# Kernel optimization log

Measured on AMD Instinct MI355X. Metric: run time of the kernel, lower is better.

## Reference

```python
import jax, jax.numpy as jnp
import numpy as np

N_NODES = 50000
N_EDGES = 150000
N_TRIS = 100000
F = 256
L = 4


def setup_inputs() -> dict:
    key = jax.random.key(0)
    ks = jax.random.split(key, 8)
    x = jax.random.normal(ks[0], (N_EDGES, F), dtype=jnp.float32)
    edge_nodes = jax.random.randint(ks[1], (N_EDGES, 2), 0, N_NODES)
    tri_edges = jax.random.randint(ks[2], (N_TRIS, 3), 0, N_EDGES)
    tri_signs = (jax.random.randint(ks[3], (N_TRIS, 3), 0, 2) * 2 - 1).astype(jnp.int32)
    std = float(np.sqrt(2.0 / (F + F)))  # xavier_uniform-equivalent std
    W0_stack = jax.random.normal(ks[4], (L, F, F), dtype=jnp.float32) * std
    W1_stack = jax.random.normal(ks[5], (L, F, F), dtype=jnp.float32) * std
    W2_stack = jax.random.normal(ks[6], (L, F, F), dtype=jnp.float32) * std
    W0_L = jax.random.normal(ks[7], (F, 1), dtype=jnp.float32) * float(np.sqrt(2.0 / (F + 1)))
    return {"x": x, "W0_stack": W0_stack, "W1_stack": W1_stack, "W2_stack": W2_stack,
            "W0_L": W0_L, "edge_nodes": edge_nodes, "tri_edges": tri_edges, "tri_signs": tri_signs}


def _b1_mm(edge_nodes, y):
    # B1 @ y : [E,F] -> [N,F];  B1[u,e] = -1, B1[v,e] = +1
    u, v = edge_nodes[:, 0], edge_nodes[:, 1]
    out = jnp.zeros((N_NODES, y.shape[1]), y.dtype)
    return out.at[u].add(-y).at[v].add(y)


def _b1t_mm(edge_nodes, z):
    # B1.T @ z : [N,F] -> [E,F]
    return z[edge_nodes[:, 1]] - z[edge_nodes[:, 0]]


def _b2t_mm(tri_edges, signs, y):
    # B2.T @ y : [E,F] -> [T,F]
    return jnp.einsum('tkf,tk->tf', y[tri_edges], signs)


def _b2_mm(tri_edges, signs, w):
    # B2 @ w : [T,F] -> [E,F]
    contrib = w[:, None, :] * signs[:, :, None]  # [T,3,F]
    out = jnp.zeros((N_EDGES, w.shape[1]), w.dtype)
    return out.at[tri_edges.reshape(-1)].add(contrib.reshape(-1, w.shape[1]))


def reference(x, W0_stack, W1_stack, W2_stack, W0_L, edge_nodes, tri_edges, tri_signs):
    signs = tri_signs.astype(x.dtype)
    for i in range(L):
        d2 = _b2_mm(tri_edges, signs, _b2t_mm(tri_edges, signs, x @ W2_stack[i]))
        d1 = x @ W1_stack[i]
        d0 = _b1t_mm(edge_nodes, _b1_mm(edge_nodes, x @ W0_stack[i]))
        x = jax.nn.relu(d2 + d1 + d0)
    return _b1_mm(edge_nodes, x @ W0_L)  # [N_NODES, 1]
```

## Files before the change

### kernel.cpp

```cpp
#include <hip/hip_runtime.h>

#define M_EDGES 150000
#define NN_NODES 50000
#define N_TRIS  100000
#define F 256
#define NLAYERS 4

#define T0 1172
#define T1 391
#define T2 782
#define NTILES (T0 + T1 + T2)
#define NT_PAD 2352
#define TPX 294

typedef __attribute__((ext_vector_type(8))) __bf16 bf16x8;
typedef __attribute__((ext_vector_type(4))) float f32x4;

__device__ inline unsigned short f2bf(float f) {
    unsigned int u = __float_as_uint(f);
    u += 0x7fff + ((u >> 16) & 1);
    return (unsigned short)(u >> 16);
}
__device__ inline float bf2f(unsigned short h) {
    return __uint_as_float(((unsigned int)h) << 16);
}

__device__ inline void async16(const void* g, void* l) {
    __builtin_amdgcn_global_load_lds(
        (const __attribute__((address_space(1))) void*)g,
        (__attribute__((address_space(3))) void*)l, 16, 0, 0);
}

__global__ __launch_bounds__(512) void gemm_mfma(
    const unsigned short* __restrict__ xb,
    const unsigned short* __restrict__ sb,
    const unsigned short* __restrict__ qb,
    const unsigned short* __restrict__ wt,
    unsigned short* __restrict__ y1,
    unsigned short* __restrict__ zb,
    unsigned short* __restrict__ wb)
{
    __shared__ unsigned short As[128 * 32];
    __shared__ unsigned short Bs[256 * 32];

    const int b    = blockIdx.x;
    const int xcd  = b & 7;
    const int idx  = b >> 3;
    const int tile = xcd * TPX + idx;
    if (tile >= NTILES) return;

    int seg, tloc;
    if (tile < T0)            { seg = 0; tloc = tile; }
    else if (tile < T0 + T1)  { seg = 1; tloc = tile - T0; }
    else                      { seg = 2; tloc = tile - T0 - T1; }
    const unsigned short* Asrc = (seg == 0) ? xb : (seg == 1) ? sb : qb;
    const int nrows = (seg == 0) ? M_EDGES : (seg == 1) ? NN_NODES : N_TRIS;
    const unsigned short* wsel = wt + seg * 65536;
    unsigned short* dst = (seg == 0) ? y1 : (seg == 1) ? zb : wb;

    const int tid  = threadIdx.x;
    const int bm0  = tloc * 128;
    const int wid  = tid >> 6;
    const int lane = tid & 63;
    const int lm   = lane & 15;
    const int lh   = lane >> 4;
    const int wm   = wid >> 2;
    const int wn   = wid & 3;
    const int wbase = tid & ~63;

    f32x4 cacc[4][4];
#pragma unroll
    for (int i = 0; i < 4; i++)
#pragma unroll
        for (int j = 0; j < 4; j++) cacc[i][j] = (f32x4){0.f, 0.f, 0.f, 0.f};

    for (int k0 = 0; k0 < 256; k0 += 32) {
        {
            int row = tid >> 2;
            int g   = (tid & 3) ^ ((row >> 1) & 3);
            int gr  = bm0 + row;
            if (gr > nrows - 1) gr = nrows - 1;
            async16(Asrc + (size_t)gr * 256 + k0 + g * 8,
                    As + (size_t)wbase * 8);
        }
#pragma unroll
        for (int ss = 0; ss < 2; ss++) {
            int i   = ss * 512 + tid;
            int row = i >> 2;
            int g   = (i & 3) ^ ((row >> 1) & 3);
            async16(wsel + (size_t)row * 256 + k0 + g * 8,
                    Bs + (size_t)(ss * 512 + wbase) * 8);
        }
        asm volatile("s_waitcnt vmcnt(0)" ::: "memory");
        __syncthreads();

        bf16x8 a[4], bfr[4];
#pragma unroll
        for (int i = 0; i < 4; i++) {
            int rr = wm * 64 + i * 16 + lm;
            a[i] = *(const bf16x8*)(As + rr * 32 + ((lh ^ ((rr >> 1) & 3)) * 8));
        }
#pragma unroll
        for (int j = 0; j < 4; j++) {
            int rr = wn * 64 + j * 16 + lm;
            bfr[j] = *(const bf16x8*)(Bs + rr * 32 + ((lh ^ ((rr >> 1) & 3)) * 8));
        }
#pragma unroll
        for (int i = 0; i < 4; i++)
#pragma unroll
            for (int j = 0; j < 4; j++)
                cacc[i][j] = __builtin_amdgcn_mfma_f32_16x16x32_bf16(
                    bfr[j], a[i], cacc[i][j], 0, 0, 0);
        __syncthreads();
    }

#pragma unroll
    for (int i = 0; i < 4; i++) {
        int grow = bm0 + wm * 64 + i * 16 + lm;
        if (grow < nrows) {
#pragma unroll
            for (int j = 0; j < 4; j++) {
                int col = wn * 64 + j * 16 + lh * 4;
                ushort4 r;
                r.x = f2bf(cacc[i][j][0]);
                r.y = f2bf(cacc[i][j][1]);
                r.z = f2bf(cacc[i][j][2]);
                r.w = f2bf(cacc[i][j][3]);
                *(ushort4*)(dst + (size_t)grow * 256 + col) = r;
            }
        }
    }
}

__global__ __launch_bounds__(256) void count_nodes(
    const int* __restrict__ en, int* __restrict__ cnt)
{
    int e = blockIdx.x * 256 + threadIdx.x;
    if (e < M_EDGES) {
        atomicAdd(&cnt[en[2 * e]], 1);
        atomicAdd(&cnt[en[2 * e + 1]], 1);
    }
}

__global__ __launch_bounds__(256) void count_tris(
    const int* __restrict__ te, int* __restrict__ cnt)
{
    int t = blockIdx.x * 256 + threadIdx.x;
    if (t < N_TRIS) {
#pragma unroll
        for (int k = 0; k < 3; k++) atomicAdd(&cnt[te[3 * t + k]], 1);
    }
}

__global__ __launch_bounds__(256) void scan_block(
    const int* __restrict__ cnt, int* __restrict__ off,
    int* __restrict__ partial, int n)
{
    __shared__ int s[256];
    int t = threadIdx.x;
    int gid = blockIdx.x * 256 + t;
    int v = (gid < n) ? cnt[gid] : 0;
    s[t] = v;
    __syncthreads();
    for (int o = 1; o < 256; o <<= 1) {
        int x = (t >= o) ? s[t - o] : 0;
        __syncthreads();
        s[t] += x;
        __syncthreads();
    }
    if (gid < n) off[gid] = s[t] - v;
    if (t == 255) partial[blockIdx.x] = s[255];
}

__global__ __launch_bounds__(1024) void scan_partial(int* __restrict__ partial, int nb)
{
    __shared__ int s[1024];
    int t = threadIdx.x;
    int v = (t < nb) ? partial[t] : 0;
    s[t] = v;
    __syncthreads();
    for (int o = 1; o < 1024; o <<= 1) {
        int x = (t >= o) ? s[t - o] : 0;
        __syncthreads();
        s[t] += x;
        __syncthreads();
    }
    if (t < nb) partial[t] = s[t] - v;
}

__global__ __launch_bounds__(256) void scan_add(
    int* __restrict__ off, int* __restrict__ cursor,
    const int* __restrict__ partial, int n, int total)
{
    int gid = blockIdx.x * 256 + threadIdx.x;
    if (gid == 0) off[n] = total;
    if (gid < n) {
        int o = off[gid] + partial[blockIdx.x];
        off[gid] = o;
        cursor[gid] = o;
    }
}

__global__ __launch_bounds__(256) void fill_nodes(
    const int* __restrict__ en, int* __restrict__ cursor, int* __restrict__ adj)
{
    int e = blockIdx.x * 256 + threadIdx.x;
    if (e < M_EDGES) {
        int u = en[2 * e], v = en[2 * e + 1];
        adj[atomicAdd(&cursor[u], 1)] = (e << 1);
        adj[atomicAdd(&cursor[v], 1)] = (e << 1) | 1;
    }
}

__global__ __launch_bounds__(256) void fill_tris(
    const int* __restrict__ te, const int* __restrict__ ts,
    int* __restrict__ cursor, int* __restrict__ adj)
{
    int t = blockIdx.x * 256 + threadIdx.x;
    if (t < N_TRIS) {
#pragma unroll
        for (int k = 0; k < 3; k++) {
            int e = te[3 * t + k];
            int neg = (ts[3 * t + k] < 0) ? 1 : 0;
            adj[atomicAdd(&cursor[e], 1)] = (t << 1) | neg;
        }
    }
}

#define ZN_BLOCKS (NN_NODES / 4)
#define WT_BLOCKS (N_TRIS / 4)

__global__ __launch_bounds__(256) void agg_fused(
    const unsigned short* __restrict__ xb,
    const int* __restrict__ noff,
    const int* __restrict__ nadj,
    unsigned short* __restrict__ sbuf,
    const int* __restrict__ te,
    const int* __restrict__ ts,
    unsigned short* __restrict__ qbuf)
{
    int lane = threadIdx.x & 63;
    int f = lane * 4;
    if (blockIdx.x < ZN_BLOCKS) {
        int n = blockIdx.x * 4 + (threadIdx.x >> 6);
        int beg = noff[n], end = noff[n + 1];
        float ax = 0.f, ay = 0.f, az = 0.f, aw = 0.f;
        int i = beg;
        for (; i + 1 < end; i += 2) {
            int ea = nadj[i], eb = nadj[i + 1];
            float sa = (ea & 1) ? 1.f : -1.f;
            float sgb = (eb & 1) ? 1.f : -1.f;
            ushort4 va = *(const ushort4*)(xb + (size_t)(ea >> 1) * 256 + f);
            ushort4 vb = *(const ushort4*)(xb + (size_t)(eb >> 1) * 256 + f);
            ax += sa * bf2f(va.x) + sgb * bf2f(vb.x);
            ay += sa * bf2f(va.y) + sgb * bf2f(vb.y);
            az += sa * bf2f(va.z) + sgb * bf2f(vb.z);
            aw += sa * bf2f(va.w) + sgb * bf2f(vb.w);
        }
        if (i < end) {
            int ea = nadj[i];
            float sa = (ea & 1) ? 1.f : -1.f;
            ushort4 va = *(const ushort4*)(xb + (size_t)(ea >> 1) * 256 + f);
            ax += sa * bf2f(va.x);
            ay += sa * bf2f(va.y);
            az += sa * bf2f(va.z);
            aw += sa * bf2f(va.w);
        }
        ushort4 r;
        r.x = f2bf(ax); r.y = f2bf(ay); r.z = f2bf(az); r.w = f2bf(aw);
        *(ushort4*)(sbuf + (size_t)n * 256 + f) = r;
    } else {
        int t = (blockIdx.x - ZN_BLOCKS) * 4 + (threadIdx.x >> 6);
        int e0 = te[3 * t + 0], e1 = te[3 * t + 1], e2 = te[3 * t + 2];
        float s0 = (float)ts[3 * t + 0];
        float s1 = (float)ts[3 * t + 1];
        float s2 = (float)ts[3 * t + 2];
        ushort4 a4 = *(const ushort4*)(xb + (size_t)e0 * 256 + f);
        ushort4 b4 = *(const ushort4*)(xb + (size_t)e1 * 256 + f);
        ushort4 d4 = *(const ushort4*)(xb + (size_t)e2 * 256 + f);
        ushort4 r;
        r.x = f2bf(s0 * bf2f(a4.x) + s1 * bf2f(b4.x) + s2 * bf2f(d4.x));
        r.y = f2bf(s0 * bf2f(a4.y) + s1 * bf2f(b4.y) + s2 * bf2f(d4.y));
        r.z = f2bf(s0 * bf2f(a4.z) + s1 * bf2f(b4.z) + s2 * bf2f(d4.z));
        r.w = f2bf(s0 * bf2f(a4.w) + s1 * bf2f(b4.w) + s2 * bf2f(d4.w));
        *(ushort4*)(qbuf + (size_t)t * 256 + f) = r;
    }
}

__global__ __launch_bounds__(256) void relu_fused(
    const unsigned short* __restrict__ y1,
    const unsigned short* __restrict__ w,
    const unsigned short* __restrict__ z,
    const int* __restrict__ en,
    const int* __restrict__ eoff,
    const int* __restrict__ eadj,
    unsigned short* __restrict__ xb,
    const float* __restrict__ wl,
    float* __restrict__ p,
    int last)
{
    int e = blockIdx.x * 4 + (threadIdx.x >> 6);
    int lane = threadIdx.x & 63;
    int f = lane * 4;
    int u = en[2 * e], v = en[2 * e + 1];
    int beg = eoff[e], end = eoff[e + 1];
    ushort4 a4 = *(const ushort4*)(y1 + (size_t)e * 256 + f);
    ushort4 zv = *(const ushort4*)(z + (size_t)v * 256 + f);
    ushort4 zu = *(const ushort4*)(z + (size_t)u * 256 + f);
    float sx = bf2f(a4.x) + bf2f(zv.x) - bf2f(zu.x);
    float sy = bf2f(a4.y) + bf2f(zv.y) - bf2f(zu.y);
    float sz = bf2f(a4.z) + bf2f(zv.z) - bf2f(zu.z);
    float sw = bf2f(a4.w) + bf2f(zv.w) - bf2f(zu.w);
    int i = beg;
    for (; i + 1 < end; i += 2) {
        int ta = eadj[i], tb = eadj[i + 1];
        float sa = (ta & 1) ? -1.f : 1.f;
        float sgb = (tb & 1) ? -1.f : 1.f;
        ushort4 wa = *(const ushort4*)(w + (size_t)(ta >> 1) * 256 + f);
        ushort4 wbv = *(const ushort4*)(w + (size_t)(tb >> 1) * 256 + f);
        sx += sa * bf2f(wa.x) + sgb * bf2f(wbv.x);
        sy += sa * bf2f(wa.y) + sgb * bf2f(wbv.y);
        sz += sa * bf2f(wa.z) + sgb * bf2f(wbv.z);
        sw += sa * bf2f(wa.w) + sgb * bf2f(wbv.w);
    }
    if (i < end) {
        int ta = eadj[i];
        float sa = (ta & 1) ? -1.f : 1.f;
        ushort4 wa = *(const ushort4*)(w + (size_t)(ta >> 1) * 256 + f);
        sx += sa * bf2f(wa.x);
        sy += sa * bf2f(wa.y);
        sz += sa * bf2f(wa.z);
        sw += sa * bf2f(wa.w);
    }
    sx = fmaxf(sx, 0.f);
    sy = fmaxf(sy, 0.f);
    sz = fmaxf(sz, 0.f);
    sw = fmaxf(sw, 0.f);
    if (!last) {
        ushort4 r;
        r.x = f2bf(sx); r.y = f2bf(sy); r.z = f2bf(sz); r.w = f2bf(sw);
        *(ushort4*)(xb + (size_t)e * 256 + f) = r;
    } else {
        float4 wv = *(const float4*)(wl + f);
        float s = sx * wv.x + sy * wv.y + sz * wv.z + sw * wv.w;
#pragma unroll
        for (int off = 32; off > 0; off >>= 1)
            s += __shfl_down(s, off, 64);
        if (lane == 0) p[e] = s;
    }
}

__global__ __launch_bounds__(256) void out_nodes(
    const float* __restrict__ p,
    const int* __restrict__ noff,
    const int* __restrict__ nadj,
    float* __restrict__ out)
{
    int n = blockIdx.x * 256 + threadIdx.x;
    if (n >= NN_NODES) return;
    int beg = noff[n], end = noff[n + 1];
    float s = 0.f;
    for (int i = beg; i < end; i++) {
        int ent = nadj[i];
        float sg = (ent & 1) ? 1.f : -1.f;
        s += sg * p[ent >> 1];
    }
    out[n] = s;
}

__global__ __launch_bounds__(256) void cvt_x(
    const float* __restrict__ x, unsigned short* __restrict__ xb)
{
    int idx = blockIdx.x * 256 + threadIdx.x;
    float4 v = *(const float4*)(x + (size_t)idx * 4);
    ushort4 r;
    r.x = f2bf(v.x); r.y = f2bf(v.y); r.z = f2bf(v.z); r.w = f2bf(v.w);
    *(ushort4*)(xb + (size_t)idx * 4) = r;
}

__global__ __launch_bounds__(256) void cvt_w(
    const float* __restrict__ W0, const float* __restrict__ W1,
    const float* __restrict__ W2, unsigned short* __restrict__ wt)
{
    int idx = blockIdx.x * 256 + threadIdx.x;
    int l = idx / (3 * 65536);
    int rem = idx - l * (3 * 65536);
    int seg = rem >> 16;
    int n = (rem >> 8) & 255;
    int k = rem & 255;
    const float* src = (seg == 0) ? W1 : (seg == 1) ? W0 : W2;
    wt[idx] = f2bf(src[(size_t)l * 65536 + k * 256 + n]);
}

extern "C" void kernel_launch(void* const* d_in, const int* in_sizes, int n_in,
                              void* d_out, int out_size, void* d_ws, size_t ws_size,
                              hipStream_t stream)
{
    const float* x0  = (const float*)d_in[0];
    const float* W0s = (const float*)d_in[1];
    const float* W1s = (const float*)d_in[2];
    const float* W2s = (const float*)d_in[3];
    const float* WL  = (const float*)d_in[4];
    const int*   en  = (const int*)d_in[5];
    const int*   te  = (const int*)d_in[6];
    const int*   ts  = (const int*)d_in[7];
    float* out = (float*)d_out;

    const size_t MF = (size_t)M_EDGES * F;
    unsigned short* xb = (unsigned short*)d_ws;
    unsigned short* y1 = xb + MF;
    unsigned short* sbuf = y1 + MF;
    unsigned short* qbuf = sbuf + (size_t)NN_NODES * 256;
    unsigned short* wt = qbuf + (size_t)N_TRIS * 256;
    unsigned short* wb = wt + (size_t)4 * 3 * 65536;
    unsigned short* zb = wb + (size_t)N_TRIS * 256;
    float* p = (float*)(zb + (size_t)NN_NODES * 256);
    int* noff = (int*)(p + M_EDGES);
    int* ncur = noff + (NN_NODES + 1);
    int* nadj = ncur + NN_NODES;
    int* eoff = nadj + 2 * M_EDGES;
    int* ecur = eoff + (M_EDGES + 1);
    int* eadj = ecur + M_EDGES;
    int* part = eadj + 3 * N_TRIS;

    cvt_w<<<(4 * 3 * 65536) / 256, 256, 0, stream>>>(W0s, W1s, W2s, wt);
    cvt_x<<<(int)(MF / 4 / 256), 256, 0, stream>>>(x0, xb);

    const int nbN = (NN_NODES + 255) / 256;
    const int nbE = (M_EDGES + 255) / 256;
    hipMemsetAsync(ncur, 0, NN_NODES * sizeof(int), stream);
    hipMemsetAsync(ecur, 0, M_EDGES * sizeof(int), stream);
    count_nodes<<<nbE, 256, 0, stream>>>(en, ncur);
    count_tris<<<(N_TRIS + 255) / 256, 256, 0, stream>>>(te, ecur);
    scan_block<<<nbN, 256, 0, stream>>>(ncur, noff, part, NN_NODES);
    scan_partial<<<1, 1024, 0, stream>>>(part, nbN);
    scan_add<<<nbN, 256, 0, stream>>>(noff, ncur, part, NN_NODES, 2 * M_EDGES);
    fill_nodes<<<nbE, 256, 0, stream>>>(en, ncur, nadj);
    scan_block<<<nbE, 256, 0, stream>>>(ecur, eoff, part, M_EDGES);
    scan_partial<<<1, 1024, 0, stream>>>(part, nbE);
    scan_add<<<nbE, 256, 0, stream>>>(eoff, ecur, part, M_EDGES, 3 * N_TRIS);
    fill_tris<<<(N_TRIS + 255) / 256, 256, 0, stream>>>(te, ts, ecur, eadj);

    for (int l = 0; l < NLAYERS; l++) {
        agg_fused<<<ZN_BLOCKS + WT_BLOCKS, 256, 0, stream>>>(
            xb, noff, nadj, sbuf, te, ts, qbuf);
        gemm_mfma<<<NT_PAD, 512, 0, stream>>>(
            xb, sbuf, qbuf, wt + (size_t)l * 3 * 65536, y1, zb, wb);
        relu_fused<<<M_EDGES / 4, 256, 0, stream>>>(
            y1, wb, zb, en, eoff, eadj, xb, WL, p, (l == NLAYERS - 1) ? 1 : 0);
    }

    out_nodes<<<(NN_NODES + 255) / 256, 256, 0, stream>>>(p, noff, nadj, out);
}
```

Baseline: 1.241 ms.

## Fuse edge GEMM with ReLU aggregation epilogue and split node/triangle GEMM

The combined three-segment GEMM becomes two kernels. One computes the node and triangle projections (z, w). The other computes the edge projection and then runs the gather, sum and ReLU epilogue directly from a swizzled LDS staging of the output tile. This removes the y1 intermediate buffer's write and read to global memory and one kernel launch per layer. The cost is 64KB of LDS per block and an epilogue where each wave walks 16 edges serially. That epilogue is likely more latency-bound than the old standalone relu kernel, which ran one edge per wave. xb is updated in place, which is safe because each block reads only its own rows before writing them.

Result: faster. 1.205 ms (-2.9%).

```diff
diff --git a/kernel.cpp b/kernel.cpp
--- a/kernel.cpp
+++ b/kernel.cpp
@@ -9,9 +9,9 @@
 #define T0 1172
 #define T1 391
 #define T2 782
-#define NTILES (T0 + T1 + T2)
-#define NT_PAD 2352
-#define TPX 294
+#define TZW (T1 + T2)
+#define GR_PAD 1176
+#define TPX8 147
 
 typedef __attribute__((ext_vector_type(8))) __bf16 bf16x8;
 typedef __attribute__((ext_vector_type(4))) float f32x4;
@@ -31,12 +31,53 @@
         (__attribute__((address_space(3))) void*)l, 16, 0, 0);
 }
 
-__global__ __launch_bounds__(512) void gemm_mfma(
-    const unsigned short* __restrict__ xb,
+
+#define GEMM_KLOOP(Asrc, wsel, nrows)                                       \
+    for (int k0 = 0; k0 < 256; k0 += 32) {                                  \
+        {                                                                   \
+            int row = tid >> 2;                                             \
+            int g   = (tid & 3) ^ ((row >> 1) & 3);                         \
+            int gr  = bm0 + row;                                            \
+            if (gr > (nrows) - 1) gr = (nrows) - 1;                         \
+            async16((Asrc) + (size_t)gr * 256 + k0 + g * 8,                 \
+                    As + (size_t)wbase * 8);                                \
+        }                                                                   \
+        _Pragma("unroll")                                                   \
+        for (int ss = 0; ss < 2; ss++) {                                    \
+            int i   = ss * 512 + tid;                                       \
+            int row = i >> 2;                                               \
+            int g   = (i & 3) ^ ((row >> 1) & 3);                           \
+            async16((wsel) + (size_t)row * 256 + k0 + g * 8,                \
+                    Bs + (size_t)(ss * 512 + wbase) * 8);                   \
+        }                                                                   \
+        asm volatile("s_waitcnt vmcnt(0)" ::: "memory");                    \
+        __syncthreads();                                                    \
+        bf16x8 a[4], bfr[4];                                                \
+        _Pragma("unroll")                                                   \
+        for (int i = 0; i < 4; i++) {                                       \
+            int rr = wm * 64 + i * 16 + lm;                                 \
+            a[i] = *(const bf16x8*)(As + rr * 32 +                          \
+                                    ((lh ^ ((rr >> 1) & 3)) * 8));          \
+        }                                                                   \
+        _Pragma("unroll")                                                   \
+        for (int j = 0; j < 4; j++) {                                       \
+            int rr = wn * 64 + j * 16 + lm;                                 \
+            bfr[j] = *(const bf16x8*)(Bs + rr * 32 +                        \
+                                      ((lh ^ ((rr >> 1) & 3)) * 8));        \
+        }                                                                   \
+        _Pragma("unroll")                                                   \
+        for (int i = 0; i < 4; i++)                                         \
+            _Pragma("unroll")                                               \
+            for (int j = 0; j < 4; j++)                                     \
+                cacc[i][j] = __builtin_amdgcn_mfma_f32_16x16x32_bf16(       \
+                    bfr[j], a[i], cacc[i][j], 0, 0, 0);                     \
+        __syncthreads();                                                    \
+    }
+
+__global__ __launch_bounds__(512) void gemm_zw(
     const unsigned short* __restrict__ sb,
     const unsigned short* __restrict__ qb,
     const unsigned short* __restrict__ wt,
-    unsigned short* __restrict__ y1,
     unsigned short* __restrict__ zb,
     unsigned short* __restrict__ wb)
 {
@@ -44,19 +85,16 @@
     __shared__ unsigned short Bs[256 * 32];
 
     const int b    = blockIdx.x;
-    const int xcd  = b & 7;
-    const int idx  = b >> 3;
-    const int tile = xcd * TPX + idx;
-    if (tile >= NTILES) return;
+    const int tile = (b & 7) * TPX8 + (b >> 3);
+    if (tile >= TZW) return;
 
     int seg, tloc;
-    if (tile < T0)            { seg = 0; tloc = tile; }
-    else if (tile < T0 + T1)  { seg = 1; tloc = tile - T0; }
-    else                      { seg = 2; tloc = tile - T0 - T1; }
-    const unsigned short* Asrc = (seg == 0) ? xb : (seg == 1) ? sb : qb;
-    const int nrows = (seg == 0) ? M_EDGES : (seg == 1) ? NN_NODES : N_TRIS;
+    if (tile < T1) { seg = 1; tloc = tile; }
+    else           { seg = 2; tloc = tile - T1; }
+    const unsigned short* Asrc = (seg == 1) ? sb : qb;
+    const int nrows = (seg == 1) ? NN_NODES : N_TRIS;
     const unsigned short* wsel = wt + seg * 65536;
-    unsigned short* dst = (seg == 0) ? y1 : (seg == 1) ? zb : wb;
+    unsigned short* dst = (seg == 1) ? zb : wb;
 
     const int tid  = threadIdx.x;
     const int bm0  = tloc * 128;
@@ -74,45 +112,7 @@
 #pragma unroll
         for (int j = 0; j < 4; j++) cacc[i][j] = (f32x4){0.f, 0.f, 0.f, 0.f};
 
-    for (int k0 = 0; k0 < 256; k0 += 32) {
-        {
-            int row = tid >> 2;
-            int g   = (tid & 3) ^ ((row >> 1) & 3);
-            int gr  = bm0 + row;
-            if (gr > nrows - 1) gr = nrows - 1;
-            async16(Asrc + (size_t)gr * 256 + k0 + g * 8,
-                    As + (size_t)wbase * 8);
-        }
-#pragma unroll
-        for (int ss = 0; ss < 2; ss++) {
-            int i   = ss * 512 + tid;
-            int row = i >> 2;
-            int g   = (i & 3) ^ ((row >> 1) & 3);
-            async16(wsel + (size_t)row * 256 + k0 + g * 8,
-                    Bs + (size_t)(ss * 512 + wbase) * 8);
-        }
-        asm volatile("s_waitcnt vmcnt(0)" ::: "memory");
-        __syncthreads();
-
-        bf16x8 a[4], bfr[4];
-#pragma unroll
-        for (int i = 0; i < 4; i++) {
-            int rr = wm * 64 + i * 16 + lm;
-            a[i] = *(const bf16x8*)(As + rr * 32 + ((lh ^ ((rr >> 1) & 3)) * 8));
-        }
-#pragma unroll
-        for (int j = 0; j < 4; j++) {
-            int rr = wn * 64 + j * 16 + lm;
-            bfr[j] = *(const bf16x8*)(Bs + rr * 32 + ((lh ^ ((rr >> 1) & 3)) * 8));
-        }
-#pragma unroll
-        for (int i = 0; i < 4; i++)
-#pragma unroll
-            for (int j = 0; j < 4; j++)
-                cacc[i][j] = __builtin_amdgcn_mfma_f32_16x16x32_bf16(
-                    bfr[j], a[i], cacc[i][j], 0, 0, 0);
-        __syncthreads();
-    }
+    GEMM_KLOOP(Asrc, wsel, nrows)
 
 #pragma unroll
     for (int i = 0; i < 4; i++) {
@@ -128,6 +128,116 @@
                 r.w = f2bf(cacc[i][j][3]);
                 *(ushort4*)(dst + (size_t)grow * 256 + col) = r;
             }
+        }
+    }
+}
+
+__global__ __launch_bounds__(512) void gemm_y1_relu(
+    unsigned short* __restrict__ xb,
+    const unsigned short* __restrict__ wt,
+    const unsigned short* __restrict__ wb,
+    const unsigned short* __restrict__ zb,
+    const int* __restrict__ en,
+    const int* __restrict__ eoff,
+    const int* __restrict__ eadj,
+    const float* __restrict__ wl,
+    float* __restrict__ p,
+    int last)
+{
+    __shared__ __align__(16) unsigned short smem[128 * 256];
+    unsigned short* const As = smem;
+    unsigned short* const Bs = smem + 128 * 32;
+
+    const int b    = blockIdx.x;
+    const int tile = (b & 7) * TPX8 + (b >> 3);
+    if (tile >= T0) return;
+
+    const int tid  = threadIdx.x;
+    const int bm0  = tile * 128;
+    const int wid  = tid >> 6;
+    const int lane = tid & 63;
+    const int lm   = lane & 15;
+    const int lh   = lane >> 4;
+    const int wm   = wid >> 2;
+    const int wn   = wid & 3;
+    const int wbase = tid & ~63;
+
+    f32x4 cacc[4][4];
+#pragma unroll
+    for (int i = 0; i < 4; i++)
+#pragma unroll
+        for (int j = 0; j < 4; j++) cacc[i][j] = (f32x4){0.f, 0.f, 0.f, 0.f};
+
+    GEMM_KLOOP(xb, wt, M_EDGES)
+
+#pragma unroll
+    for (int i = 0; i < 4; i++) {
+        int lr  = wm * 64 + i * 16 + lm;
+        int key = (lr & 7) << 4;
+#pragma unroll
+        for (int j = 0; j < 4; j++) {
+            int colb = wn * 128 + j * 32 + lh * 8;
+            ushort4 r;
+            r.x = f2bf(cacc[i][j][0]);
+            r.y = f2bf(cacc[i][j][1]);
+            r.z = f2bf(cacc[i][j][2]);
+            r.w = f2bf(cacc[i][j][3]);
+            *(ushort4*)((char*)smem + (size_t)lr * 512 + (colb ^ key)) = r;
+        }
+    }
+    __syncthreads();
+
+    const int f = lane * 4;
+    for (int r8 = 0; r8 < 16; r8++) {
+        int lr = r8 * 8 + wid;
+        int e  = bm0 + lr;
+        if (e >= M_EDGES) break;
+        ushort4 yv = *(const ushort4*)((const char*)smem + (size_t)lr * 512 +
+                                       ((lane * 8) ^ ((lr & 7) << 4)));
+        int u = en[2 * e], v = en[2 * e + 1];
+        ushort4 zv4 = *(const ushort4*)(zb + (size_t)v * 256 + f);
+        ushort4 zu4 = *(const ushort4*)(zb + (size_t)u * 256 + f);
+        float sx = bf2f(yv.x) + bf2f(zv4.x) - bf2f(zu4.x);
+        float sy = bf2f(yv.y) + bf2f(zv4.y) - bf2f(zu4.y);
+        float sz = bf2f(yv.z) + bf2f(zv4.z) - bf2f(zu4.z);
+        float sw = bf2f(yv.w) + bf2f(zv4.w) - bf2f(zu4.w);
+        int beg = eoff[e], end = eoff[e + 1];
+        int i2 = beg;
+        for (; i2 + 1 < end; i2 += 2) {
+            int ta = eadj[i2], tb = eadj[i2 + 1];
+            float sa  = (ta & 1) ? -1.f : 1.f;
+            float sgb = (tb & 1) ? -1.f : 1.f;
+            ushort4 wa  = *(const ushort4*)(wb + (size_t)(ta >> 1) * 256 + f);
+            ushort4 wbv = *(const ushort4*)(wb + (size_t)(tb >> 1) * 256 + f);
+            sx += sa * bf2f(wa.x) + sgb * bf2f(wbv.x);
+            sy += sa * bf2f(wa.y) + sgb * bf2f(wbv.y);
+            sz += sa * bf2f(wa.z) + sgb * bf2f(wbv.z);
+            sw += sa * bf2f(wa.w) + sgb * bf2f(wbv.w);
+        }
+        if (i2 < end) {
+            int ta = eadj[i2];
+            float sa = (ta & 1) ? -1.f : 1.f;
+            ushort4 wa = *(const ushort4*)(wb + (size_t)(ta >> 1) * 256 + f);
+            sx += sa * bf2f(wa.x);
+            sy += sa * bf2f(wa.y);
+            sz += sa * bf2f(wa.z);
+            sw += sa * bf2f(wa.w);
+        }
+        sx = fmaxf(sx, 0.f);
+        sy = fmaxf(sy, 0.f);
+        sz = fmaxf(sz, 0.f);
+        sw = fmaxf(sw, 0.f);
+        if (!last) {
+            ushort4 r;
+            r.x = f2bf(sx); r.y = f2bf(sy); r.z = f2bf(sz); r.w = f2bf(sw);
+            *(ushort4*)(xb + (size_t)e * 256 + f) = r;
+        } else {
+            float4 wv = *(const float4*)(wl + f);
+            float s = sx * wv.x + sy * wv.y + sz * wv.z + sw * wv.w;
+#pragma unroll
+            for (int off = 32; off > 0; off >>= 1)
+                s += __shfl_down(s, off, 64);
+            if (lane == 0) p[e] = s;
         }
     }
 }
@@ -287,69 +397,6 @@
     }
 }
 
-__global__ __launch_bounds__(256) void relu_fused(
-    const unsigned short* __restrict__ y1,
-    const unsigned short* __restrict__ w,
-    const unsigned short* __restrict__ z,
-    const int* __restrict__ en,
-    const int* __restrict__ eoff,
-    const int* __restrict__ eadj,
-    unsigned short* __restrict__ xb,
-    const float* __restrict__ wl,
-    float* __restrict__ p,
-    int last)
-{
-    int e = blockIdx.x * 4 + (threadIdx.x >> 6);
-    int lane = threadIdx.x & 63;
-    int f = lane * 4;
-    int u = en[2 * e], v = en[2 * e + 1];
-    int beg = eoff[e], end = eoff[e + 1];
-    ushort4 a4 = *(const ushort4*)(y1 + (size_t)e * 256 + f);
-    ushort4 zv = *(const ushort4*)(z + (size_t)v * 256 + f);
-    ushort4 zu = *(const ushort4*)(z + (size_t)u * 256 + f);
-    float sx = bf2f(a4.x) + bf2f(zv.x) - bf2f(zu.x);
-    float sy = bf2f(a4.y) + bf2f(zv.y) - bf2f(zu.y);
-    float sz = bf2f(a4.z) + bf2f(zv.z) - bf2f(zu.z);
-    float sw = bf2f(a4.w) + bf2f(zv.w) - bf2f(zu.w);
-    int i = beg;
-    for (; i + 1 < end; i += 2) {
-        int ta = eadj[i], tb = eadj[i + 1];
-        float sa = (ta & 1) ? -1.f : 1.f;
-        float sgb = (tb & 1) ? -1.f : 1.f;
-        ushort4 wa = *(const ushort4*)(w + (size_t)(ta >> 1) * 256 + f);
-        ushort4 wbv = *(const ushort4*)(w + (size_t)(tb >> 1) * 256 + f);
-        sx += sa * bf2f(wa.x) + sgb * bf2f(wbv.x);
-        sy += sa * bf2f(wa.y) + sgb * bf2f(wbv.y);
-        sz += sa * bf2f(wa.z) + sgb * bf2f(wbv.z);
-        sw += sa * bf2f(wa.w) + sgb * bf2f(wbv.w);
-    }
-    if (i < end) {
-        int ta = eadj[i];
-        float sa = (ta & 1) ? -1.f : 1.f;
-        ushort4 wa = *(const ushort4*)(w + (size_t)(ta >> 1) * 256 + f);
-        sx += sa * bf2f(wa.x);
-        sy += sa * bf2f(wa.y);
-        sz += sa * bf2f(wa.z);
-        sw += sa * bf2f(wa.w);
-    }
-    sx = fmaxf(sx, 0.f);
-    sy = fmaxf(sy, 0.f);
-    sz = fmaxf(sz, 0.f);
-    sw = fmaxf(sw, 0.f);
-    if (!last) {
-        ushort4 r;
-        r.x = f2bf(sx); r.y = f2bf(sy); r.z = f2bf(sz); r.w = f2bf(sw);
-        *(ushort4*)(xb + (size_t)e * 256 + f) = r;
-    } else {
-        float4 wv = *(const float4*)(wl + f);
-        float s = sx * wv.x + sy * wv.y + sz * wv.z + sw * wv.w;
-#pragma unroll
-        for (int off = 32; off > 0; off >>= 1)
-            s += __shfl_down(s, off, 64);
-        if (lane == 0) p[e] = s;
-    }
-}
-
 __global__ __launch_bounds__(256) void out_nodes(
     const float* __restrict__ p,
     const int* __restrict__ noff,
@@ -444,10 +491,11 @@
     for (int l = 0; l < NLAYERS; l++) {
         agg_fused<<<ZN_BLOCKS + WT_BLOCKS, 256, 0, stream>>>(
             xb, noff, nadj, sbuf, te, ts, qbuf);
-        gemm_mfma<<<NT_PAD, 512, 0, stream>>>(
-            xb, sbuf, qbuf, wt + (size_t)l * 3 * 65536, y1, zb, wb);
-        relu_fused<<<M_EDGES / 4, 256, 0, stream>>>(
-            y1, wb, zb, en, eoff, eadj, xb, WL, p, (l == NLAYERS - 1) ? 1 : 0);
+        gemm_zw<<<GR_PAD, 512, 0, stream>>>(
+            sbuf, qbuf, wt + (size_t)l * 3 * 65536, zb, wb);
+        gemm_y1_relu<<<GR_PAD, 512, 0, stream>>>(
+            xb, wt + (size_t)l * 3 * 65536, wb, zb, en, eoff, eadj,
+            WL, p, (l == NLAYERS - 1) ? 1 : 0);
     }
 
     out_nodes<<<(NN_NODES + 255) / 256, 256, 0, stream>>>(p, noff, nadj, out);
```

## Fuse edge GEMM with ReLU epilogue and split node/tri GEMM

Applied to the files above, without the earlier changes.

The x@W1 GEMM for edges moves out of the combined GEMM into a new kernel with 64-row tiles. That kernel stages the bf16 result in swizzled LDS and then applies the gather of z/w, the ReLU and the output write in place. This removes the y1 round trip through global memory and one kernel launch per layer. The node/triangle GEMMs now run in a smaller kernel of their own. Separately, node aggregation loads up to 64 adjacency entries per wave at once and broadcasts them with shuffles instead of reading them one by one. The risks are a lower-occupancy GEMM with a larger LDS footprint, and the in-place update of xb, which relies on each block reading only its own rows.

After: 1.210 ms. 1.03x faster.

```diff
diff --git a/kernel.cpp b/kernel.cpp
--- a/kernel.cpp
+++ b/kernel.cpp
@@ -6,12 +6,13 @@
 #define F 256
 #define NLAYERS 4
 
-#define T0 1172
 #define T1 391
 #define T2 782
-#define NTILES (T0 + T1 + T2)
-#define NT_PAD 2352
-#define TPX 294
+#define TZW (T1 + T2)
+#define ZW_PAD 1176
+#define TPXZW 147
+#define T0_64 2344
+#define TPX64 293
 
 typedef __attribute__((ext_vector_type(8))) __bf16 bf16x8;
 typedef __attribute__((ext_vector_type(4))) float f32x4;
@@ -31,12 +32,11 @@
         (__attribute__((address_space(3))) void*)l, 16, 0, 0);
 }
 
-__global__ __launch_bounds__(512) void gemm_mfma(
-    const unsigned short* __restrict__ xb,
+
+__global__ __launch_bounds__(512) void gemm_zw(
     const unsigned short* __restrict__ sb,
     const unsigned short* __restrict__ qb,
     const unsigned short* __restrict__ wt,
-    unsigned short* __restrict__ y1,
     unsigned short* __restrict__ zb,
     unsigned short* __restrict__ wb)
 {
@@ -44,19 +44,16 @@
     __shared__ unsigned short Bs[256 * 32];
 
     const int b    = blockIdx.x;
-    const int xcd  = b & 7;
-    const int idx  = b >> 3;
-    const int tile = xcd * TPX + idx;
-    if (tile >= NTILES) return;
+    const int tile = (b & 7) * TPXZW + (b >> 3);
+    if (tile >= TZW) return;
 
     int seg, tloc;
-    if (tile < T0)            { seg = 0; tloc = tile; }
-    else if (tile < T0 + T1)  { seg = 1; tloc = tile - T0; }
-    else                      { seg = 2; tloc = tile - T0 - T1; }
-    const unsigned short* Asrc = (seg == 0) ? xb : (seg == 1) ? sb : qb;
-    const int nrows = (seg == 0) ? M_EDGES : (seg == 1) ? NN_NODES : N_TRIS;
+    if (tile < T1) { seg = 1; tloc = tile; }
+    else           { seg = 2; tloc = tile - T1; }
+    const unsigned short* Asrc = (seg == 1) ? sb : qb;
+    const int nrows = (seg == 1) ? NN_NODES : N_TRIS;
     const unsigned short* wsel = wt + seg * 65536;
-    unsigned short* dst = (seg == 0) ? y1 : (seg == 1) ? zb : wb;
+    unsigned short* dst = (seg == 1) ? zb : wb;
 
     const int tid  = threadIdx.x;
     const int bm0  = tloc * 128;
@@ -132,6 +129,181 @@
     }
 }
 
+__global__ __launch_bounds__(256) void gemm_y1_relu(
+    unsigned short* __restrict__ xb,
+    const unsigned short* __restrict__ wt,
+    const unsigned short* __restrict__ wb,
+    const unsigned short* __restrict__ zb,
+    const int* __restrict__ en,
+    const int* __restrict__ eoff,
+    const int* __restrict__ eadj,
+    const float* __restrict__ wl,
+    float* __restrict__ p,
+    int last)
+{
+    __shared__ __align__(16) unsigned short smem[64 * 256];
+    unsigned short* const As = smem;
+    unsigned short* const Bs = smem + 64 * 32;
+
+    const int b    = blockIdx.x;
+    const int tile = (b & 7) * TPX64 + (b >> 3);
+
+    const int tid  = threadIdx.x;
+    const int bm0  = tile * 64;
+    const int wid  = tid >> 6;
+    const int lane = tid & 63;
+    const int lm   = lane & 15;
+    const int lh   = lane >> 4;
+    const int wn   = wid;
+    const int wbase = tid & ~63;
+
+    f32x4 cacc[4][4];
+#pragma unroll
+    for (int i = 0; i < 4; i++)
+#pragma unroll
+        for (int j = 0; j < 4; j++) cacc[i][j] = (f32x4){0.f, 0.f, 0.f, 0.f};
+
+    for (int k0 = 0; k0 < 256; k0 += 32) {
+        {
+            int row = tid >> 2;
+            int g   = (tid & 3) ^ ((row >> 1) & 3);
+            int gr  = bm0 + row;
+            if (gr > M_EDGES - 1) gr = M_EDGES - 1;
+            async16(xb + (size_t)gr * 256 + k0 + g * 8,
+                    As + (size_t)wbase * 8);
+        }
+#pragma unroll
+        for (int ss = 0; ss < 4; ss++) {
+            int i   = ss * 256 + tid;
+            int row = i >> 2;
+            int g   = (i & 3) ^ ((row >> 1) & 3);
+            async16(wt + (size_t)row * 256 + k0 + g * 8,
+                    Bs + (size_t)(ss * 256 + wbase) * 8);
+        }
+        asm volatile("s_waitcnt vmcnt(0)" ::: "memory");
+        __syncthreads();
+
+        bf16x8 a[4], bfr[4];
+#pragma unroll
+        for (int i = 0; i < 4; i++) {
+            int rr = i * 16 + lm;
+            a[i] = *(const bf16x8*)(As + rr * 32 + ((lh ^ ((rr >> 1) & 3)) * 8));
+        }
+#pragma unroll
+        for (int j = 0; j < 4; j++) {
+            int rr = wn * 64 + j * 16 + lm;
+            bfr[j] = *(const bf16x8*)(Bs + rr * 32 + ((lh ^ ((rr >> 1) & 3)) * 8));
+        }
+#pragma unroll
+        for (int i = 0; i < 4; i++)
+#pragma unroll
+            for (int j = 0; j < 4; j++)
+                cacc[i][j] = __builtin_amdgcn_mfma_f32_16x16x32_bf16(
+                    bfr[j], a[i], cacc[i][j], 0, 0, 0);
+        __syncthreads();
+    }
+
+#pragma unroll
+    for (int i = 0; i < 4; i++) {
+        int lr  = i * 16 + lm;
+        int key = (lr & 7) << 4;
+#pragma unroll
+        for (int j = 0; j < 4; j++) {
+            int colb = wn * 128 + j * 32 + lh * 8;
+            ushort4 r;
+            r.x = f2bf(cacc[i][j][0]);
+            r.y = f2bf(cacc[i][j][1]);
+            r.z = f2bf(cacc[i][j][2]);
+            r.w = f2bf(cacc[i][j][3]);
+            *(ushort4*)((char*)smem + (size_t)lr * 512 + (colb ^ key)) = r;
+        }
+    }
+    __syncthreads();
+
+    const int f = lane * 4;
+    for (int k = 0; k < 8; k++) {
+        int lr0 = k * 8 + wid;
+        int lr1 = lr0 + 4;
+        int e0  = bm0 + lr0;
+        if (e0 >= M_EDGES) break;
+        int e1  = bm0 + lr1;
+        int ok1 = (e1 < M_EDGES);
+        int e1c = ok1 ? e1 : (M_EDGES - 1);
+
+        ushort4 yv0 = *(const ushort4*)((const char*)smem + (size_t)lr0 * 512 +
+                                        ((lane * 8) ^ ((lr0 & 7) << 4)));
+        ushort4 yv1 = *(const ushort4*)((const char*)smem + (size_t)lr1 * 512 +
+                                        ((lane * 8) ^ ((lr1 & 7) << 4)));
+        int u0 = en[2 * e0], v0 = en[2 * e0 + 1];
+        int u1 = en[2 * e1c], v1 = en[2 * e1c + 1];
+        ushort4 zv0 = *(const ushort4*)(zb + (size_t)v0 * 256 + f);
+        ushort4 zu0 = *(const ushort4*)(zb + (size_t)u0 * 256 + f);
+        ushort4 zv1 = *(const ushort4*)(zb + (size_t)v1 * 256 + f);
+        ushort4 zu1 = *(const ushort4*)(zb + (size_t)u1 * 256 + f);
+        int beg0 = eoff[e0], end0 = eoff[e0 + 1];
+        int beg1 = eoff[e1c], end1 = eoff[e1c + 1];
+
+        float s0x = bf2f(yv0.x) + bf2f(zv0.x) - bf2f(zu0.x);
+        float s0y = bf2f(yv0.y) + bf2f(zv0.y) - bf2f(zu0.y);
+        float s0z = bf2f(yv0.z) + bf2f(zv0.z) - bf2f(zu0.z);
+        float s0w = bf2f(yv0.w) + bf2f(zv0.w) - bf2f(zu0.w);
+        float s1x = bf2f(yv1.x) + bf2f(zv1.x) - bf2f(zu1.x);
+        float s1y = bf2f(yv1.y) + bf2f(zv1.y) - bf2f(zu1.y);
+        float s1z = bf2f(yv1.z) + bf2f(zv1.z) - bf2f(zu1.z);
+        float s1w = bf2f(yv1.w) + bf2f(zv1.w) - bf2f(zu1.w);
+
+        for (int i2 = beg0; i2 < end0; i2++) {
+            int ta = eadj[i2];
+            float sa = (ta & 1) ? -1.f : 1.f;
+            ushort4 wa = *(const ushort4*)(wb + (size_t)(ta >> 1) * 256 + f);
+            s0x += sa * bf2f(wa.x);
+            s0y += sa * bf2f(wa.y);
+            s0z += sa * bf2f(wa.z);
+            s0w += sa * bf2f(wa.w);
+        }
+        for (int i2 = beg1; i2 < end1; i2++) {
+            int ta = eadj[i2];
+            float sa = (ta & 1) ? -1.f : 1.f;
+            ushort4 wa = *(const ushort4*)(wb + (size_t)(ta >> 1) * 256 + f);
+            s1x += sa * bf2f(wa.x);
+            s1y += sa * bf2f(wa.y);
+            s1z += sa * bf2f(wa.z);
+            s1w += sa * bf2f(wa.w);
+        }
+
+        s0x = fmaxf(s0x, 0.f); s0y = fmaxf(s0y, 0.f);
+        s0z = fmaxf(s0z, 0.f); s0w = fmaxf(s0w, 0.f);
+        s1x = fmaxf(s1x, 0.f); s1y = fmaxf(s1y, 0.f);
+        s1z = fmaxf(s1z, 0.f); s1w = fmaxf(s1w, 0.f);
+
+        if (!last) {
+            ushort4 r0;
+            r0.x = f2bf(s0x); r0.y = f2bf(s0y);
+            r0.z = f2bf(s0z); r0.w = f2bf(s0w);
+            *(ushort4*)(xb + (size_t)e0 * 256 + f) = r0;
+            if (ok1) {
+                ushort4 r1;
+                r1.x = f2bf(s1x); r1.y = f2bf(s1y);
+                r1.z = f2bf(s1z); r1.w = f2bf(s1w);
+                *(ushort4*)(xb + (size_t)e1 * 256 + f) = r1;
+            }
+        } else {
+            float4 wv = *(const float4*)(wl + f);
+            float d0 = s0x * wv.x + s0y * wv.y + s0z * wv.z + s0w * wv.w;
+            float d1 = s1x * wv.x + s1y * wv.y + s1z * wv.z + s1w * wv.w;
+#pragma unroll
+            for (int off = 32; off > 0; off >>= 1) {
+                d0 += __shfl_down(d0, off, 64);
+                d1 += __shfl_down(d1, off, 64);
+            }
+            if (lane == 0) {
+                p[e0] = d0;
+                if (ok1) p[e1] = d1;
+            }
+        }
+    }
+}
+
 __global__ __launch_bounds__(256) void count_nodes(
     const int* __restrict__ en, int* __restrict__ cnt)
 {
@@ -244,10 +416,16 @@
     if (blockIdx.x < ZN_BLOCKS) {
         int n = blockIdx.x * 4 + (threadIdx.x >> 6);
         int beg = noff[n], end = noff[n + 1];
+        int deg = end - beg;
+        int cl = beg + lane;
+        if (cl > 2 * M_EDGES - 1) cl = 2 * M_EDGES - 1;
+        int entL = nadj[cl];
+        int dmax = (deg < 64) ? deg : 64;
         float ax = 0.f, ay = 0.f, az = 0.f, aw = 0.f;
-        int i = beg;
-        for (; i + 1 < end; i += 2) {
-            int ea = nadj[i], eb = nadj[i + 1];
+        int j = 0;
+        for (; j + 1 < dmax; j += 2) {
+            int ea = __shfl(entL, j, 64);
+            int eb = __shfl(entL, j + 1, 64);
             float sa = (ea & 1) ? 1.f : -1.f;
             float sgb = (eb & 1) ? 1.f : -1.f;
             ushort4 va = *(const ushort4*)(xb + (size_t)(ea >> 1) * 256 + f);
@@ -257,7 +435,16 @@
             az += sa * bf2f(va.z) + sgb * bf2f(vb.z);
             aw += sa * bf2f(va.w) + sgb * bf2f(vb.w);
         }
-        if (i < end) {
+        if (j < dmax) {
+            int ea = __shfl(entL, j, 64);
+            float sa = (ea & 1) ? 1.f : -1.f;
+            ushort4 va = *(const ushort4*)(xb + (size_t)(ea >> 1) * 256 + f);
+            ax += sa * bf2f(va.x);
+            ay += sa * bf2f(va.y);
+            az += sa * bf2f(va.z);
+            aw += sa * bf2f(va.w);
+        }
+        for (int i = beg + 64; i < end; i++) {
             int ea = nadj[i];
             float sa = (ea & 1) ? 1.f : -1.f;
             ushort4 va = *(const ushort4*)(xb + (size_t)(ea >> 1) * 256 + f);
@@ -287,69 +474,6 @@
     }
 }
 
-__global__ __launch_bounds__(256) void relu_fused(
-    const unsigned short* __restrict__ y1,
-    const unsigned short* __restrict__ w,
-    const unsigned short* __restrict__ z,
-    const int* __restrict__ en,
-    const int* __restrict__ eoff,
-    const int* __restrict__ eadj,
-    unsigned short* __restrict__ xb,
-    const float* __restrict__ wl,
-    float* __restrict__ p,
-    int last)
-{
-    int e = blockIdx.x * 4 + (threadIdx.x >> 6);
-    int lane = threadIdx.x & 63;
-    int f = lane * 4;
-    int u = en[2 * e], v = en[2 * e + 1];
-    int beg = eoff[e], end = eoff[e + 1];
-    ushort4 a4 = *(const ushort4*)(y1 + (size_t)e * 256 + f);
-    ushort4 zv = *(const ushort4*)(z + (size_t)v * 256 + f);
-    ushort4 zu = *(const ushort4*)(z + (size_t)u * 256 + f);
-    float sx = bf2f(a4.x) + bf2f(zv.x) - bf2f(zu.x);
-    float sy = bf2f(a4.y) + bf2f(zv.y) - bf2f(zu.y);
-    float sz = bf2f(a4.z) + bf2f(zv.z) - bf2f(zu.z);
-    float sw = bf2f(a4.w) + bf2f(zv.w) - bf2f(zu.w);
-    int i = beg;
-    for (; i + 1 < end; i += 2) {
-        int ta = eadj[i], tb = eadj[i + 1];
-        float sa = (ta & 1) ? -1.f : 1.f;
-        float sgb = (tb & 1) ? -1.f : 1.f;
-        ushort4 wa = *(const ushort4*)(w + (size_t)(ta >> 1) * 256 + f);
-        ushort4 wbv = *(const ushort4*)(w + (size_t)(tb >> 1) * 256 + f);
-        sx += sa * bf2f(wa.x) + sgb * bf2f(wbv.x);
-        sy += sa * bf2f(wa.y) + sgb * bf2f(wbv.y);
-        sz += sa * bf2f(wa.z) + sgb * bf2f(wbv.z);
-        sw += sa * bf2f(wa.w) + sgb * bf2f(wbv.w);
-    }
-    if (i < end) {
-        int ta = eadj[i];
-        float sa = (ta & 1) ? -1.f : 1.f;
-        ushort4 wa = *(const ushort4*)(w + (size_t)(ta >> 1) * 256 + f);
-        sx += sa * bf2f(wa.x);
-        sy += sa * bf2f(wa.y);
-        sz += sa * bf2f(wa.z);
-        sw += sa * bf2f(wa.w);
-    }
-    sx = fmaxf(sx, 0.f);
-    sy = fmaxf(sy, 0.f);
-    sz = fmaxf(sz, 0.f);
-    sw = fmaxf(sw, 0.f);
-    if (!last) {
-        ushort4 r;
-        r.x = f2bf(sx); r.y = f2bf(sy); r.z = f2bf(sz); r.w = f2bf(sw);
-        *(ushort4*)(xb + (size_t)e * 256 + f) = r;
-    } else {
-        float4 wv = *(const float4*)(wl + f);
-        float s = sx * wv.x + sy * wv.y + sz * wv.z + sw * wv.w;
-#pragma unroll
-        for (int off = 32; off > 0; off >>= 1)
-            s += __shfl_down(s, off, 64);
-        if (lane == 0) p[e] = s;
-    }
-}
-
 __global__ __launch_bounds__(256) void out_nodes(
     const float* __restrict__ p,
     const int* __restrict__ noff,
@@ -444,10 +568,11 @@
     for (int l = 0; l < NLAYERS; l++) {
         agg_fused<<<ZN_BLOCKS + WT_BLOCKS, 256, 0, stream>>>(
             xb, noff, nadj, sbuf, te, ts, qbuf);
-        gemm_mfma<<<NT_PAD, 512, 0, stream>>>(
-            xb, sbuf, qbuf, wt + (size_t)l * 3 * 65536, y1, zb, wb);
-        relu_fused<<<M_EDGES / 4, 256, 0, stream>>>(
-            y1, wb, zb, en, eoff, eadj, xb, WL, p, (l == NLAYERS - 1) ? 1 : 0);
+        gemm_zw<<<ZW_PAD, 512, 0, stream>>>(
+            sbuf, qbuf, wt + (size_t)l * 3 * 65536, zb, wb);
+        gemm_y1_relu<<<T0_64, 256, 0, stream>>>(
+            xb, wt + (size_t)l * 3 * 65536, wb, zb, en, eoff, eadj,
+            WL, p, (l == NLAYERS - 1) ? 1 : 0);
     }
 
     out_nodes<<<(NN_NODES + 255) / 256, 256, 0, stream>>>(p, noff, nadj, out);
```
